# Performance work log

Hardware: AMD Instinct MI355X
Metric: run time of the kernel (lower is better)

The kernel has to match this reference:

```python
import jax, jax.numpy as jnp
import numpy as np

B, L, S, D, H, CTX = 2, 2048, 512, 1024, 16, 1024
HD = D // H
HID = 4 * D
EPS = 1e-6


def _ln(x):
    mu = jnp.mean(x, axis=-1, keepdims=True)
    var = jnp.mean((x - mu) ** 2, axis=-1, keepdims=True)
    return (x - mu) * jax.lax.rsqrt(var + EPS)


def _rotate_half(x):
    x1, x2 = jnp.split(x, 2, axis=-1)
    return jnp.concatenate([-x2, x1], axis=-1)


def _heads(t):  # [B,N,D] -> [B,H,N,HD]
    return t.reshape(t.shape[0], t.shape[1], H, HD).transpose(0, 2, 1, 3)


def _merge(t):  # [B,H,N,HD] -> [B,N,D]
    return t.transpose(0, 2, 1, 3).reshape(t.shape[0], t.shape[2], D)


def setup_inputs() -> dict:
    key = jax.random.key(0)
    ks = jax.random.split(key, 24)
    s = 0.02
    inp = {
        "x": jax.random.normal(ks[0], (B, L, D), jnp.float32),
        "timestep_emb": jax.random.normal(ks[1], (B, D), jnp.float32),
        "context_emb": jax.random.normal(ks[2], (B, S, CTX), jnp.float32),
        "rope_emb": jax.random.normal(ks[3], (L, HD), jnp.float32),
        # adaLN modulation: Linear(D -> 6D) with bias
        "w_mod": jax.random.normal(ks[4], (D, 6 * D), jnp.float32) * s,
        "b_mod": jnp.zeros((6 * D,), jnp.float32),
        # self-attention (no qkv bias, out has bias)
        "wq_s": jax.random.normal(ks[5], (D, D), jnp.float32) * s,
        "wk_s": jax.random.normal(ks[6], (D, D), jnp.float32) * s,
        "wv_s": jax.random.normal(ks[7], (D, D), jnp.float32) * s,
        "wo_s": jax.random.normal(ks[8], (D, D), jnp.float32) * s,
        "bo_s": jnp.zeros((D,), jnp.float32),
        # cross-attention (q/k/v no bias, out has bias)
        "wq_c": jax.random.normal(ks[9], (D, D), jnp.float32) * s,
        "wk_c": jax.random.normal(ks[10], (CTX, D), jnp.float32) * s,
        "wv_c": jax.random.normal(ks[11], (CTX, D), jnp.float32) * s,
        "wo_c": jax.random.normal(ks[12], (D, D), jnp.float32) * s,
        "bo_c": jnp.zeros((D,), jnp.float32),
        # MLP
        "w1": jax.random.normal(ks[13], (D, HID), jnp.float32) * s,
        "b1": jnp.zeros((HID,), jnp.float32),
        "w2": jax.random.normal(ks[14], (HID, D), jnp.float32) * s,
        "b2": jnp.zeros((D,), jnp.float32),
    }
    return inp


def reference(x, timestep_emb, context_emb, rope_emb,
              w_mod, b_mod,
              wq_s, wk_s, wv_s, wo_s, bo_s,
              wq_c, wk_c, wv_c, wo_c, bo_c,
              w1, b1, w2, b2):
    scale = HD ** -0.5
    # adaLN modulation from timestep embedding
    mods = jnp.split(timestep_emb @ w_mod + b_mod, 6, axis=-1)
    shift_msa, scale_msa, gate_msa, shift_mlp, scale_mlp, gate_mlp = mods

    # --- self-attention with RoPE ---
    nx = _ln(x) * (1.0 + scale_msa[:, None, :]) + shift_msa[:, None, :]
    q = _heads(nx @ wq_s)
    k = _heads(nx @ wk_s)
    v = _heads(nx @ wv_s)
    cos = jnp.cos(rope_emb)[None, None]  # [1,1,L,HD]
    sin = jnp.sin(rope_emb)[None, None]
    q = q * cos + _rotate_half(q) * sin
    k = k * cos + _rotate_half(k) * sin
    attn = jax.nn.softmax(jnp.einsum("bhqd,bhkd->bhqk", q, k) * scale, axis=-1)
    sa = _merge(jnp.einsum("bhqk,bhkd->bhqd", attn, v)) @ wo_s + bo_s
    x = x + gate_msa[:, None, :] * sa

    # --- cross-attention (no mask) ---
    nx = _ln(x)
    q = _heads(nx @ wq_c)
    k = _heads(context_emb @ wk_c)
    v = _heads(context_emb @ wv_c)
    attn = jax.nn.softmax(jnp.einsum("bhqd,bhkd->bhqk", q, k) * scale, axis=-1)
    ca = _merge(jnp.einsum("bhqk,bhkd->bhqd", attn, v)) @ wo_c + bo_c
    x = x + ca

    # --- MLP with modulation + gate ---
    nx = _ln(x) * (1.0 + scale_mlp[:, None, :]) + shift_mlp[:, None, :]
    h = jax.nn.gelu(nx @ w1 + b1, approximate=False)
    x = x + gate_mlp[:, None, :] * (h @ w2 + b2)
    return x
```

## Files before the change

kernel.cpp:

```cpp
#include <hip/hip_runtime.h>
#include <hip/hip_bf16.h>


typedef short short8 __attribute__((ext_vector_type(8)));
typedef float f32x4 __attribute__((ext_vector_type(4)));
typedef float f32x16 __attribute__((ext_vector_type(16)));

#define DEV __device__ __forceinline__

DEV unsigned short f2b(float f) {
  __hip_bfloat16 h = __float2bfloat16(f);
  return *reinterpret_cast<unsigned short*>(&h);
}
DEV float b2f(unsigned short u) {
  unsigned int x = ((unsigned int)u) << 16;
  return __builtin_bit_cast(float, x);
}
DEV unsigned int pk2(float lo, float hi) {
  unsigned int r;
  asm("v_cvt_pk_bf16_f32 %0, %1, %2" : "=v"(r) : "v"(lo), "v"(hi));
  return r;
}
DEV void vpsw(unsigned int& a, unsigned int& b) {
  asm("v_permlane32_swap_b32 %0, %1" : "+v"(a), "+v"(b));
}
DEV float max3f(float a, float b, float c) {
  float r;
  asm("v_max3_f32 %0, %1, %2, %3" : "=v"(r) : "v"(a), "v"(b), "v"(c));
  return r;
}

#define GLB(p) ((const __attribute__((address_space(1))) void*)(p))
#define LDSP(p) ((__attribute__((address_space(3))) void*)(p))

__global__ __launch_bounds__(256) void transpose_cast(
    const float* __restrict__ in, unsigned short* __restrict__ out, int R, int C,
    float scale) {
  __shared__ float tile[32][33];
  int bx = blockIdx.x * 32, by = blockIdx.y * 32;
  int tx = threadIdx.x, ty = threadIdx.y;
#pragma unroll
  for (int i = ty; i < 32; i += 8)
    tile[i][tx] = in[(size_t)(by + i) * C + bx + tx];
  __syncthreads();
#pragma unroll
  for (int i = ty; i < 32; i += 8)
    out[(size_t)(bx + i) * R + by + tx] = f2b(tile[tx][i] * scale);
}

struct TCB { const float* in; unsigned short* out; float scale; };
struct TC8 { TCB m[8]; };
__global__ __launch_bounds__(256) void transpose_cast8(TC8 a) {
  __shared__ float tile[32][33];
  const float* in = a.m[blockIdx.z].in;
  unsigned short* out = a.m[blockIdx.z].out;
  float scale = a.m[blockIdx.z].scale;
  int bx = blockIdx.x * 32, by = blockIdx.y * 32;
  int tx = threadIdx.x, ty = threadIdx.y;
#pragma unroll
  for (int i = ty; i < 32; i += 8)
    tile[i][tx] = in[(size_t)(by + i) * 1024 + bx + tx];
  __syncthreads();
#pragma unroll
  for (int i = ty; i < 32; i += 8)
    out[(size_t)(bx + i) * 1024 + by + tx] = f2b(tile[tx][i] * scale);
}

__global__ __launch_bounds__(256) void cast_bf16(
    const float* __restrict__ in, unsigned short* __restrict__ out, int n) {
  int i = blockIdx.x * 256 + threadIdx.x;
  if (i < n) out[i] = f2b(in[i]);
}

__global__ __launch_bounds__(256) void rope_tab(
    const float* __restrict__ rope, float* __restrict__ cosT, float* __restrict__ sinT, int n) {
  int i = blockIdx.x * 256 + threadIdx.x;
  if (i < n) {
    float v = rope[i];
    cosT[i] = cosf(v);
    sinT[i] = sinf(v);
  }
}

__global__ __launch_bounds__(256) void mods_kernel(
    const float* __restrict__ te, const unsigned short* __restrict__ wmodT,
    const float* __restrict__ bmod, float* __restrict__ mods) {
  int w = blockIdx.x * 4 + (threadIdx.x >> 6);
  int lane = threadIdx.x & 63;
  int b = w / 6144, j = w % 6144;
  const unsigned short* wr = wmodT + (size_t)j * 1024;
  const float* ter = te + (size_t)b * 1024;
  int k0 = lane * 16;
  float sum = 0.f;
#pragma unroll
  for (int u = 0; u < 2; ++u) {
    short8 wv = *(const short8*)(wr + k0 + u * 8);
#pragma unroll
    for (int e = 0; e < 8; ++e)
      sum += b2f((unsigned short)wv[e]) * ter[k0 + u * 8 + e];
  }
#pragma unroll
  for (int off = 32; off >= 1; off >>= 1) sum += __shfl_down(sum, off);
  if (lane == 0) mods[(size_t)b * 6144 + j] = sum + bmod[j];
}

__global__ __launch_bounds__(256) void ln_mod(
    const float* __restrict__ x, const float* __restrict__ mods,
    unsigned short* __restrict__ out, int scale_ofs, int shift_ofs) {
  int row = blockIdx.x;
  int b = row >> 11;
  int tid = threadIdx.x;
  const float* xr = x + (size_t)row * 1024;
  float4 v = ((const float4*)xr)[tid];
  float s = v.x + v.y + v.z + v.w;
  float ss = v.x * v.x + v.y * v.y + v.z * v.z + v.w * v.w;
#pragma unroll
  for (int off = 32; off >= 1; off >>= 1) {
    s += __shfl_down(s, off);
    ss += __shfl_down(ss, off);
  }
  __shared__ float red[8];
  int wave = tid >> 6, lane = tid & 63;
  if (lane == 0) { red[wave] = s; red[4 + wave] = ss; }
  __syncthreads();
  if (tid == 0) {
    float S = red[0] + red[1] + red[2] + red[3];
    float SS = red[4] + red[5] + red[6] + red[7];
    float mu = S * (1.f / 1024.f);
    red[0] = mu;
    red[1] = SS * (1.f / 1024.f) - mu * mu;
  }
  __syncthreads();
  float mu = red[0];
  float rs = rsqrtf(red[1] + 1e-6f);
  float vv[4] = {v.x, v.y, v.z, v.w};
  unsigned short o[4];
#pragma unroll
  for (int c = 0; c < 4; ++c) {
    int col = tid * 4 + c;
    float nv = (vv[c] - mu) * rs;
    if (scale_ofs >= 0)
      nv = nv * (1.f + mods[(size_t)b * 6144 + scale_ofs + col]) +
           mods[(size_t)b * 6144 + shift_ofs + col];
    o[c] = f2b(nv);
  }
  *(ushort4*)(&out[(size_t)row * 1024 + tid * 4]) = *(const ushort4*)o;
}

__global__ __launch_bounds__(256) void rope_apply(
    unsigned short* __restrict__ qb, unsigned short* __restrict__ kb,
    const float* __restrict__ cosT, const float* __restrict__ sinT) {
  int idx = blockIdx.x * 256 + threadIdx.x;
  unsigned short* buf = blockIdx.y ? kb : qb;
  int row = idx >> 9;
  int rem = idx & 511;
  int h = rem >> 5, d = rem & 31;
  int l = row & 2047;
  size_t base = (size_t)row * 1024 + h * 64 + d;
  float x1 = b2f(buf[base]), x2 = b2f(buf[base + 32]);
  float c1 = cosT[l * 64 + d], s1 = sinT[l * 64 + d];
  float c2 = cosT[l * 64 + d + 32], s2 = sinT[l * 64 + d + 32];
  buf[base] = f2b(x1 * c1 - x2 * s1);
  buf[base + 32] = f2b(x2 * c2 + x1 * s2);
}

template <int EPI, int MI, int NJ>
DEV void gemm_epilogue(f32x4 (&acc)[MI][NJ], void* Cout, const float* bias,
                       const float* mods, int gate_ofs, const float* src,
                       int N, int rowsPerB, int m0, int n0, int wm, int wn,
                       int g, int r) {
#pragma unroll
  for (int i = 0; i < MI; ++i) {
#pragma unroll
    for (int j = 0; j < NJ; ++j) {
#pragma unroll
      for (int q = 0; q < 4; ++q) {
        size_t grow = (size_t)(m0 + wm + i * 16 + g * 4 + q);
        size_t gcol = (size_t)(n0 + wn + j * 16 + r);
        float v = acc[i][j][q];
        if constexpr (EPI == 0) {
          ((unsigned short*)Cout)[grow * N + gcol] = f2b(v);
        } else if constexpr (EPI == 1) {
          v += bias[gcol];
          float ge = 0.5f * v * (1.0f + erff(v * 0.70710678f));
          ((unsigned short*)Cout)[grow * N + gcol] = f2b(ge);
        } else if constexpr (EPI == 3) {
          size_t buf = gcol >> 10;
          ((unsigned short*)Cout)[buf * (4096ull * 1024) + grow * 1024 + (gcol & 1023)] = f2b(v);
        } else {
          v += bias[gcol];
          float gate = 1.0f;
          if (gate_ofs >= 0)
            gate = mods[(grow / rowsPerB) * 6144 + gate_ofs + gcol];
          ((float*)Cout)[grow * N + gcol] = src[grow * N + gcol] + gate * v;
        }
      }
    }
  }
}

template <int EPI>
__global__ __launch_bounds__(256, 2) void gemm_bt(
    const unsigned short* __restrict__ A, const unsigned short* __restrict__ Bt,
    void* __restrict__ Cout, const float* __restrict__ bias,
    const float* __restrict__ mods, int gate_ofs, const float* __restrict__ src,
    int M, int N, int K, int rowsPerB) {
  __shared__ unsigned short As[128 * 32];
  __shared__ unsigned short Bs[128 * 32];
  const int tid = threadIdx.x;
  const int wave = tid >> 6, lane = tid & 63;
  const int g = lane >> 4, r = lane & 15;
  const int m0 = blockIdx.y * 128, n0 = blockIdx.x * 128;
  const int wm = (wave >> 1) * 64, wn = (wave & 1) * 64;
  const int srow = lane >> 2;
  const int scol = (lane & 3) * 8;

  f32x4 acc[4][4] = {};

  for (int k0 = 0; k0 < K; k0 += 32) {
    __syncthreads();
#pragma unroll
    for (int cc = 0; cc < 4; ++cc) {
      int c = wave * 4 + cc;
      int isB = c >> 3;
      int cl = c & 7;
      int row = cl * 16 + srow;
      const unsigned short* gsrc =
          isB ? (Bt + (size_t)(n0 + row) * K + k0 + scol)
              : (A + (size_t)(m0 + row) * K + k0 + scol);
      unsigned short* ldst = (isB ? Bs : As) + cl * 512;
      __builtin_amdgcn_global_load_lds(GLB(gsrc), LDSP(ldst), 16, 0, 0);
    }
    __syncthreads();

    short8 bfr[4];
#pragma unroll
    for (int j = 0; j < 4; ++j)
      bfr[j] = *(const short8*)(&Bs[(wn + j * 16 + r) * 32 + g * 8]);
#pragma unroll
    for (int i = 0; i < 4; ++i) {
      short8 af = *(const short8*)(&As[(wm + i * 16 + r) * 32 + g * 8]);
#pragma unroll
      for (int j = 0; j < 4; ++j)
        acc[i][j] = __builtin_amdgcn_mfma_f32_16x16x32_bf16(af, bfr[j], acc[i][j], 0, 0, 0);
    }
  }
  gemm_epilogue<EPI, 4, 4>(acc, Cout, bias, mods, gate_ofs, src, N, rowsPerB,
                           m0, n0, wm, wn, g, r);
}

template <int EPI>
__global__ __launch_bounds__(256) void gemm_pipe(
    const unsigned short* __restrict__ A, const unsigned short* __restrict__ Bt,
    void* __restrict__ Cout, const float* __restrict__ bias,
    const float* __restrict__ mods, int gate_ofs, const float* __restrict__ src,
    int M, int N, int K, int rowsPerB, int mshift) {
  __shared__ unsigned short lds[4 * 16384];
  const int tid = threadIdx.x;
  const int wave = tid >> 6, lane = tid & 63;
  const int g = lane >> 4, r = lane & 15;
  const int flat = blockIdx.x;
  const int xcd = flat & 7, idx = flat >> 3;
  const int mt = xcd * (1 << mshift) + (idx & ((1 << mshift) - 1));
  const int nt = idx >> mshift;
  const int m0 = mt * 128, n0 = nt * 128;
  const int wm = (wave >> 1) * 64, wn = (wave & 1) * 64;
  const int srow8 = lane >> 3;
  const int sck = (lane & 7) ^ srow8;

  f32x4 acc[4][4] = {};

  auto stage = [&](int t, int bufi) {
    const int k0 = t * 64;
#pragma unroll
    for (int i = 0; i < 8; ++i) {
      int u = wave * 8 + i;
      int isB = u >> 4;
      int uu = u & 15;
      int rl = uu * 8 + srow8;
      const unsigned short* gsrc =
          (isB ? (Bt + (size_t)(n0 + rl) * K) : (A + (size_t)(m0 + rl) * K)) +
          k0 + sck * 8;
      unsigned short* dst = (unsigned short*)lds + bufi * 16384 + isB * 8192 + uu * 512;
      __builtin_amdgcn_global_load_lds(GLB(gsrc), LDSP(dst), 16, 0, 0);
    }
  };

  const int nt_k = K / 64;
  stage(0, 0);
  stage(1, 1);
  stage(2, 2);

  for (int t = 0; t < nt_k; ++t) {
    int rem = nt_k - t;
    if (rem >= 3) {
      asm volatile("s_waitcnt vmcnt(16)" ::: "memory");
    } else if (rem == 2) {
      asm volatile("s_waitcnt vmcnt(8)" ::: "memory");
    } else {
      asm volatile("s_waitcnt vmcnt(0)" ::: "memory");
    }
    __builtin_amdgcn_sched_barrier(0);
    __builtin_amdgcn_s_barrier();
    __builtin_amdgcn_sched_barrier(0);
    if (t + 3 < nt_k) stage(t + 3, (t + 3) & 3);

    const unsigned short* Ab = (const unsigned short*)lds + (t & 3) * 16384;
    const unsigned short* Bb = Ab + 8192;
#pragma unroll
    for (int ks = 0; ks < 2; ++ks) {
      short8 bfr[4];
#pragma unroll
      for (int j = 0; j < 4; ++j) {
        int row = wn + j * 16 + r;
        bfr[j] = *(const short8*)&Bb[row * 64 + ((g + ks * 4) ^ (r & 7)) * 8];
      }
#pragma unroll
      for (int i = 0; i < 4; ++i) {
        int row = wm + i * 16 + r;
        short8 af = *(const short8*)&Ab[row * 64 + ((g + ks * 4) ^ (r & 7)) * 8];
#pragma unroll
        for (int j = 0; j < 4; ++j)
          acc[i][j] = __builtin_amdgcn_mfma_f32_16x16x32_bf16(af, bfr[j], acc[i][j], 0, 0, 0);
      }
    }
  }
  gemm_epilogue<EPI, 4, 4>(acc, Cout, bias, mods, gate_ofs, src, N, rowsPerB,
                           m0, n0, wm, wn, g, r);
}

template <int EPI>
__global__ __launch_bounds__(256) void gemm_p2(
    const unsigned short* __restrict__ A, const unsigned short* __restrict__ Bt,
    void* __restrict__ Cout, const float* __restrict__ bias,
    const float* __restrict__ mods, int gate_ofs, const float* __restrict__ src,
    int M, int N, int K, int rowsPerB, int ntn) {
  __shared__ unsigned short lds[3 * 12288];
  const int tid = threadIdx.x;
  const int wave = tid >> 6, lane = tid & 63;
  const int g = lane >> 4, r = lane & 15;
  const int flat = blockIdx.x;
  const int nt = flat % ntn, mt = flat / ntn;
  const int m0 = mt * 64, n0 = nt * 128;
  const int wm = (wave >> 1) * 32, wn = (wave & 1) * 64;
  const int srow8 = lane >> 3;
  const int sck = (lane & 7) ^ srow8;

  f32x4 acc[2][4] = {};

  auto stage = [&](int t, int bufi) {
    const int k0 = t * 64;
    unsigned short* base = (unsigned short*)lds + bufi * 12288;
#pragma unroll
    for (int i = 0; i < 2; ++i) {
      int u = wave * 2 + i;
      int rl = u * 8 + srow8;
      const unsigned short* gsrc = A + (size_t)(m0 + rl) * K + k0 + sck * 8;
      __builtin_amdgcn_global_load_lds(GLB(gsrc), LDSP(base + u * 512), 16, 0, 0);
    }
#pragma unroll
    for (int i = 0; i < 4; ++i) {
      int u = wave * 4 + i;
      int rl = u * 8 + srow8;
      const unsigned short* gsrc = Bt + (size_t)(n0 + rl) * K + k0 + sck * 8;
      __builtin_amdgcn_global_load_lds(GLB(gsrc), LDSP(base + 4096 + u * 512), 16, 0, 0);
    }
  };

  const int ntk = K / 64;
  stage(0, 0);
  stage(1, 1);
  int cbuf = 0, sbuf = 2;

  for (int t = 0; t < ntk; ++t) {
    if (t < ntk - 1) {
      asm volatile("s_waitcnt vmcnt(6)" ::: "memory");
    } else {
      asm volatile("s_waitcnt vmcnt(0)" ::: "memory");
    }
    __builtin_amdgcn_sched_barrier(0);
    __builtin_amdgcn_s_barrier();
    __builtin_amdgcn_sched_barrier(0);
    if (t + 2 < ntk) {
      stage(t + 2, sbuf);
      sbuf = (sbuf == 2) ? 0 : sbuf + 1;
    }

    const unsigned short* Ab = (const unsigned short*)lds + cbuf * 12288;
    const unsigned short* Bb = Ab + 4096;
#pragma unroll
    for (int ks = 0; ks < 2; ++ks) {
      short8 bfr[4];
#pragma unroll
      for (int j = 0; j < 4; ++j) {
        int row = wn + j * 16 + r;
        bfr[j] = *(const short8*)&Bb[row * 64 + ((g + ks * 4) ^ (r & 7)) * 8];
      }
#pragma unroll
      for (int i = 0; i < 2; ++i) {
        int row = wm + i * 16 + r;
        short8 af = *(const short8*)&Ab[row * 64 + ((g + ks * 4) ^ (r & 7)) * 8];
#pragma unroll
        for (int j = 0; j < 4; ++j)
          acc[i][j] = __builtin_amdgcn_mfma_f32_16x16x32_bf16(af, bfr[j], acc[i][j], 0, 0, 0);
      }
    }
    cbuf = (cbuf == 2) ? 0 : cbuf + 1;
  }
  gemm_epilogue<EPI, 2, 4>(acc, Cout, bias, mods, gate_ofs, src, N, rowsPerB,
                           m0, n0, wm, wn, g, r);
}

__global__ __launch_bounds__(256, 2) void flash2(
    const unsigned short* __restrict__ Q, const unsigned short* __restrict__ Kv,
    const unsigned short* __restrict__ Vv, unsigned short* __restrict__ O,
    int Lk) {
  __shared__ unsigned short lds[20480];
  const int tid = threadIdx.x, wave = tid >> 6, lane = tid & 63;
  const int hi = lane >> 5, lq = lane & 31;
  const int flat = blockIdx.x;
  const int xcd = flat & 7, rr = flat >> 3;
  const int gl = rr >> 4, qt = rr & 15;
  const int g = xcd * 4 + gl;
  const int h = g & 15, b = g >> 4;
  const int Lq = 2048, D = 1024;

  const unsigned short* Qbase =
      Q + ((size_t)b * Lq + qt * 128 + wave * 32 + lq) * D + h * 64;
  const unsigned short* Kbase = Kv + (size_t)b * Lk * D + h * 64;
  const unsigned short* Vbase = Vv + (size_t)b * Lk * D + h * 64;

  short8 qf[4];
#pragma unroll
  for (int kb = 0; kb < 4; ++kb)
    qf[kb] = *(const short8*)(Qbase + kb * 16 + hi * 8);

  const short8 ones = {0x3F80, 0x3F80, 0x3F80, 0x3F80, 0x3F80, 0x3F80, 0x3F80, 0x3F80};

  const int kr0 = tid >> 3, kc0 = tid & 7;
  const int kvp = tid >> 3, db = tid & 7;
  const int kch0 = (kc0 ^ (kr0 & 7) ^ (kr0 >> 3)) & 7;
  const int kch1 = kch0 ^ 4;
  const int f0 = (lq & 7) ^ (lq >> 3);
  const int swz0 = f0 << 4, swz1 = swz0 ^ 64;

  int vby[8];
#pragma unroll
  for (int e = 0; e < 8; ++e) {
    int d = db * 8 + e;
    vby[e] = d * 128 + ((kvp * 4) ^ (((e ^ db) & 7) << 4));
  }

  float m_run = -3.0e38f;
  f32x16 o0 = {}, o1 = {}, lacc = {};
  short8 vr0, vr1;
  short8 pbf[4];

  auto stageK = [&](int t, int bi) {
    const unsigned short* s0 = Kbase + (size_t)(t * 64 + kr0) * D + kch0 * 8;
    const unsigned short* s1 = Kbase + (size_t)(t * 64 + kr0 + 32) * D + kch1 * 8;
    __builtin_amdgcn_global_load_lds(GLB(s0), LDSP(&lds[bi * 4096 + wave * 512]), 16, 0, 0);
    __builtin_amdgcn_global_load_lds(GLB(s1), LDSP(&lds[bi * 4096 + 2048 + wave * 512]), 16, 0, 0);
  };
  auto loadV = [&](int t) {
    const unsigned short* v0 = Vbase + (size_t)(t * 64 + 2 * kvp) * D + db * 8;
    vr0 = *(const short8*)v0;
    vr1 = *(const short8*)(v0 + D);
  };
  auto writeV = [&](int t) {
    char* vt = (char*)&lds[12288 + (t & 1) * 4096];
#pragma unroll
    for (int e = 0; e < 8; ++e)
      *(unsigned int*)(vt + vby[e]) =
          (unsigned int)(unsigned short)vr0[e] |
          ((unsigned int)(unsigned short)vr1[e] << 16);
  };
  auto qk = [&](int bi, f32x16& sa0, f32x16& sa1) {
    const unsigned short* K0 = &lds[bi * 4096];
#pragma unroll
    for (int ks = 0; ks < 4; ++ks) {
      int lo = ks * 32 + hi * 16;
      short8 a0 = *(const short8*)&K0[lq * 64 + ((lo ^ swz0) >> 1)];
      short8 a1 = *(const short8*)&K0[(32 + lq) * 64 + ((lo ^ swz1) >> 1)];
      sa0 = __builtin_amdgcn_mfma_f32_32x32x16_bf16(a0, qf[ks], sa0, 0, 0, 0);
      sa1 = __builtin_amdgcn_mfma_f32_32x32x16_bf16(a1, qf[ks], sa1, 0, 0, 0);
    }
  };
  auto finish = [&](f32x16& s0a, f32x16& s1a) {
    float tm[8];
#pragma unroll
    for (int i = 0; i < 8; ++i)
      tm[i] = fmaxf(max3f(s0a[i], s0a[i + 8], s1a[i]), s1a[i + 8]);
    float x = max3f(tm[0], tm[1], tm[2]);
    float y = max3f(tm[3], tm[4], tm[5]);
    float pm = fmaxf(max3f(tm[6], tm[7], x), y);
    {
      unsigned int ua = __builtin_bit_cast(unsigned int, pm), ub = ua;
      vpsw(ua, ub);
      pm = fmaxf(__builtin_bit_cast(float, ua), __builtin_bit_cast(float, ub));
    }
    if (__any(pm - m_run > 8.0f)) {
      float mnew = fmaxf(m_run, pm);
      float alpha = exp2f(m_run - mnew);
      lacc[0] *= alpha;
#pragma unroll
      for (int i = 0; i < 16; ++i) { o0[i] *= alpha; o1[i] *= alpha; }
      m_run = mnew;
    }
    float mc = m_run;
#pragma unroll
    for (int i = 0; i < 16; ++i) s0a[i] = exp2f(s0a[i] - mc);
#pragma unroll
    for (int i = 0; i < 16; ++i) s1a[i] = exp2f(s1a[i] - mc);
#pragma unroll
    for (int kb = 0; kb < 4; ++kb) {
      int bb = (kb & 1) * 8;
      float p0, p1, p2, p3, p4, p5, p6, p7;
      if (kb < 2) {
        p0 = s0a[bb + 0]; p1 = s0a[bb + 1]; p2 = s0a[bb + 2]; p3 = s0a[bb + 3];
        p4 = s0a[bb + 4]; p5 = s0a[bb + 5]; p6 = s0a[bb + 6]; p7 = s0a[bb + 7];
      } else {
        p0 = s1a[bb + 0]; p1 = s1a[bb + 1]; p2 = s1a[bb + 2]; p3 = s1a[bb + 3];
        p4 = s1a[bb + 4]; p5 = s1a[bb + 5]; p6 = s1a[bb + 6]; p7 = s1a[bb + 7];
      }
      unsigned int u0 = pk2(p0, p1), u1 = pk2(p2, p3);
      unsigned int u2 = pk2(p4, p5), u3 = pk2(p6, p7);
      vpsw(u0, u2);
      vpsw(u1, u3);
      union { unsigned int u[4]; short8 s; } fr;
      fr.u[0] = u0; fr.u[1] = u1; fr.u[2] = u2; fr.u[3] = u3;
      pbf[kb] = fr.s;
    }
  };
  auto pv = [&](int t) {
    const unsigned short* V0 = &lds[12288 + (t & 1) * 4096];
    __builtin_amdgcn_s_setprio(1);
#pragma unroll
    for (int kb = 0; kb < 4; ++kb) {
      int lo = kb * 32 + hi * 16;
      short8 vf0 = *(const short8*)&V0[lq * 64 + ((lo ^ swz0) >> 1)];
      short8 vf1 = *(const short8*)&V0[(32 + lq) * 64 + ((lo ^ swz1) >> 1)];
      o0 = __builtin_amdgcn_mfma_f32_32x32x16_bf16(vf0, pbf[kb], o0, 0, 0, 0);
      o1 = __builtin_amdgcn_mfma_f32_32x32x16_bf16(vf1, pbf[kb], o1, 0, 0, 0);
      lacc = __builtin_amdgcn_mfma_f32_32x32x16_bf16(ones, pbf[kb], lacc, 0, 0, 0);
    }
    __builtin_amdgcn_s_setprio(0);
  };

  const int nkt = Lk / 64;

  stageK(0, 0);
  loadV(0);
  writeV(0);
  stageK(1, 1);
  __syncthreads();

  f32x16 sA0 = {}, sA1 = {}, sB0, sB1;
  qk(0, sA0, sA1);

  auto pstep = [&](int t, f32x16& n0, f32x16& n1, f32x16& p0, f32x16& p1) {
    const int tq = t + 1;
    if (tq < nkt) {
      loadV(tq);
      if (tq + 1 < nkt) stageK(tq + 1, (tq + 1) % 3);
      n0 = {}; n1 = {};
      qk(tq % 3, n0, n1);
    }
    finish(p0, p1);
    if (tq < nkt) writeV(tq);
    pv(t);
    __syncthreads();
  };

  for (int t = 0; t < nkt; t += 2) {
    pstep(t, sB0, sB1, sA0, sA1);
    pstep(t + 1, sA0, sA1, sB0, sB1);
  }

  float rl = 1.0f / lacc[0];
  unsigned short* os = &lds[wave * 2048];
#pragma unroll
  for (int t = 0; t < 2; ++t) {
#pragma unroll
    for (int c = 0; c < 4; ++c) {
      int dbase = 32 * t + 8 * c + 4 * hi;
      float v0 = (t ? o1[4 * c + 0] : o0[4 * c + 0]) * rl;
      float v1 = (t ? o1[4 * c + 1] : o0[4 * c + 1]) * rl;
      float v2 = (t ? o1[4 * c + 2] : o0[4 * c + 2]) * rl;
      float v3 = (t ? o1[4 * c + 3] : o0[4 * c + 3]) * rl;
      int by0 = lq * 128 + ((dbase * 2) ^ ((lq & 7) << 4));
      int by1 = lq * 128 + (((dbase + 2) * 2) ^ ((lq & 7) << 4));
      *(unsigned int*)((char*)os + by0) = pk2(v0, v1);
      *(unsigned int*)((char*)os + by1) = pk2(v2, v3);
    }
  }
  int q2 = lane >> 1;
  unsigned short* orow =
      O + ((size_t)b * Lq + qt * 128 + wave * 32 + q2) * D + h * 64;
#pragma unroll
  for (int j = 0; j < 4; ++j) {
    int j2 = (lane & 1) * 4 + j;
    int byr = q2 * 128 + ((j2 * 16) ^ ((q2 & 7) << 4));
    short8 vv = *(const short8*)((char*)os + byr);
    *(short8*)(orow + j2 * 8) = vv;
  }
}

extern "C" void kernel_launch(void* const* d_in, const int* in_sizes, int n_in,
                              void* d_out, int out_size, void* d_ws, size_t ws_size,
                              hipStream_t stream) {
  (void)in_sizes; (void)n_in; (void)out_size; (void)ws_size;
  const float* x_in = (const float*)d_in[0];
  const float* te   = (const float*)d_in[1];
  const float* ctx  = (const float*)d_in[2];
  const float* rope = (const float*)d_in[3];
  const float* wmod = (const float*)d_in[4];
  const float* bmod = (const float*)d_in[5];
  const float* wqs  = (const float*)d_in[6];
  const float* wks  = (const float*)d_in[7];
  const float* wvs  = (const float*)d_in[8];
  const float* wos  = (const float*)d_in[9];
  const float* bos  = (const float*)d_in[10];
  const float* wqc  = (const float*)d_in[11];
  const float* wkc  = (const float*)d_in[12];
  const float* wvc  = (const float*)d_in[13];
  const float* woc  = (const float*)d_in[14];
  const float* boc  = (const float*)d_in[15];
  const float* w1   = (const float*)d_in[16];
  const float* b1   = (const float*)d_in[17];
  const float* w2   = (const float*)d_in[18];
  const float* b2   = (const float*)d_in[19];
  float* out = (float*)d_out;

  char* w = (char*)d_ws;
  size_t o = 0;
  auto alloc = [&](size_t bytes) {
    char* p = w + o;
    o = (o + bytes + 255) & ~(size_t)255;
    return p;
  };
  unsigned short* wmodT = (unsigned short*)alloc(6144ull * 1024 * 2);
  unsigned short* wqsT  = (unsigned short*)alloc(1024ull * 1024 * 2);
  unsigned short* wksT  = (unsigned short*)alloc(1024ull * 1024 * 2);
  unsigned short* wvsT  = (unsigned short*)alloc(1024ull * 1024 * 2);
  unsigned short* wosT  = (unsigned short*)alloc(1024ull * 1024 * 2);
  unsigned short* wqcT  = (unsigned short*)alloc(1024ull * 1024 * 2);
  unsigned short* wkcT  = (unsigned short*)alloc(1024ull * 1024 * 2);
  unsigned short* wvcT  = (unsigned short*)alloc(1024ull * 1024 * 2);
  unsigned short* wocT  = (unsigned short*)alloc(1024ull * 1024 * 2);
  unsigned short* w1T   = (unsigned short*)alloc(4096ull * 1024 * 2);
  unsigned short* w2T   = (unsigned short*)alloc(1024ull * 4096 * 2);
  float* modsb = (float*)alloc(2ull * 6144 * 4);
  float* cosT  = (float*)alloc(2048ull * 64 * 4);
  float* sinT  = (float*)alloc(2048ull * 64 * 4);
  unsigned short* nx   = (unsigned short*)alloc(4096ull * 1024 * 2);
  unsigned short* ctxb = (unsigned short*)alloc(1024ull * 1024 * 2);
  unsigned short* qb = (unsigned short*)alloc(4096ull * 1024 * 2);
  unsigned short* kb = (unsigned short*)alloc(4096ull * 1024 * 2);
  unsigned short* vb = (unsigned short*)alloc(4096ull * 1024 * 2);
  unsigned short* ao = (unsigned short*)alloc(4096ull * 1024 * 2);
  float* xw = (float*)alloc(4096ull * 1024 * 4);
  unsigned short* hbuf = qb;

  const float c1 = 0.125f * 1.4426950408889634f;

  dim3 tb(32, 8);
  transpose_cast<<<dim3(6144 / 32, 1024 / 32), tb, 0, stream>>>(wmod, wmodT, 1024, 6144, 1.0f);
  TC8 tc8;
  tc8.m[0] = {wqs, wqsT, c1};
  tc8.m[1] = {wks, wksT, 1.0f};
  tc8.m[2] = {wvs, wvsT, 1.0f};
  tc8.m[3] = {wos, wosT, 1.0f};
  tc8.m[4] = {wqc, wqcT, 1.0f};
  tc8.m[5] = {wkc, wkcT, c1};
  tc8.m[6] = {wvc, wvcT, 1.0f};
  tc8.m[7] = {woc, wocT, 1.0f};
  transpose_cast8<<<dim3(32, 32, 8), tb, 0, stream>>>(tc8);
  transpose_cast<<<dim3(4096 / 32, 1024 / 32), tb, 0, stream>>>(w1, w1T, 1024, 4096, 1.0f);
  transpose_cast<<<dim3(1024 / 32, 4096 / 32), tb, 0, stream>>>(w2, w2T, 4096, 1024, 1.0f);

  cast_bf16<<<4096, 256, 0, stream>>>(ctx, ctxb, 1024 * 1024);
  rope_tab<<<512, 256, 0, stream>>>(rope, cosT, sinT, 2048 * 64);
  mods_kernel<<<3072, 256, 0, stream>>>(te, wmodT, bmod, modsb);

  ln_mod<<<4096, 256, 0, stream>>>(x_in, modsb, nx, 1024, 0);
  gemm_pipe<3><<<768, 256, 0, stream>>>(nx, wqsT, qb, nullptr, nullptr, -1, nullptr, 4096, 3072, 1024, 2048, 2);
  rope_apply<<<dim3(8192, 2), 256, 0, stream>>>(qb, kb, cosT, sinT);
  flash2<<<512, 256, 0, stream>>>(qb, kb, vb, ao, 2048);
  gemm_p2<2><<<512, 256, 0, stream>>>(ao, wosT, xw, bos, modsb, 2048, x_in, 4096, 1024, 1024, 2048, 8);

  ln_mod<<<4096, 256, 0, stream>>>(xw, modsb, nx, -1, -1);
  gemm_p2<0><<<512, 256, 0, stream>>>(nx, wqcT, qb, nullptr, nullptr, -1, nullptr, 4096, 1024, 1024, 2048, 8);
  gemm_p2<3><<<256, 256, 0, stream>>>(ctxb, wkcT, kb, nullptr, nullptr, -1, nullptr, 1024, 2048, 1024, 512, 16);
  flash2<<<512, 256, 0, stream>>>(qb, kb, vb, ao, 512);
  gemm_p2<2><<<512, 256, 0, stream>>>(ao, wocT, xw, boc, modsb, -1, xw, 4096, 1024, 1024, 2048, 8);

  ln_mod<<<4096, 256, 0, stream>>>(xw, modsb, nx, 4096, 3072);
  gemm_bt<1><<<dim3(32, 32), 256, 0, stream>>>(nx, w1T, hbuf, b1, nullptr, -1, nullptr, 4096, 4096, 1024, 2048);
  gemm_p2<2><<<512, 256, 0, stream>>>(hbuf, w2T, out, b2, modsb, 5120, xw, 4096, 1024, 4096, 2048, 8);
}
```

Baseline: 409.9 us.

## Fuse RoPE into QKV GEMM epilogue and trim flash-attention accumulator init

New measurement: 401.1 us. 2.2% less time.

```diff
diff --git a/kernel.cpp b/kernel.cpp
--- a/kernel.cpp
+++ b/kernel.cpp
@@ -73,12 +73,11 @@
 }
 
 __global__ __launch_bounds__(256) void rope_tab(
-    const float* __restrict__ rope, float* __restrict__ cosT, float* __restrict__ sinT, int n) {
+    const float* __restrict__ rope, float2* __restrict__ cs, int n) {
   int i = blockIdx.x * 256 + threadIdx.x;
   if (i < n) {
     float v = rope[i];
-    cosT[i] = cosf(v);
-    sinT[i] = sinf(v);
+    cs[i] = make_float2(cosf(v), sinf(v));
   }
 }
 
@@ -145,23 +144,6 @@
     o[c] = f2b(nv);
   }
   *(ushort4*)(&out[(size_t)row * 1024 + tid * 4]) = *(const ushort4*)o;
-}
-
-__global__ __launch_bounds__(256) void rope_apply(
-    unsigned short* __restrict__ qb, unsigned short* __restrict__ kb,
-    const float* __restrict__ cosT, const float* __restrict__ sinT) {
-  int idx = blockIdx.x * 256 + threadIdx.x;
-  unsigned short* buf = blockIdx.y ? kb : qb;
-  int row = idx >> 9;
-  int rem = idx & 511;
-  int h = rem >> 5, d = rem & 31;
-  int l = row & 2047;
-  size_t base = (size_t)row * 1024 + h * 64 + d;
-  float x1 = b2f(buf[base]), x2 = b2f(buf[base + 32]);
-  float c1 = cosT[l * 64 + d], s1 = sinT[l * 64 + d];
-  float c2 = cosT[l * 64 + d + 32], s2 = sinT[l * 64 + d + 32];
-  buf[base] = f2b(x1 * c1 - x2 * s1);
-  buf[base + 32] = f2b(x2 * c2 + x1 * s2);
 }
 
 template <int EPI, int MI, int NJ>
@@ -199,6 +181,37 @@
   }
 }
 
+DEV void qkv_rope_epilogue(f32x4 (&acc)[4][4], unsigned short* Cout,
+                           const float2* cs, int m0, int n0, int wm, int wn,
+                           int g, int r) {
+  const int buf = (n0 + wn) >> 10;
+  const int colbase = (n0 + wn) & 1023;
+  unsigned short* base = Cout + (size_t)buf * (4096ull * 1024);
+#pragma unroll
+  for (int i = 0; i < 4; ++i) {
+#pragma unroll
+    for (int q = 0; q < 4; ++q) {
+      size_t grow = (size_t)(m0 + wm + i * 16 + g * 4 + q);
+      unsigned short* orow = base + grow * 1024 + colbase + r;
+      if (buf < 2) {
+        int l = (int)(grow & 2047);
+#pragma unroll
+        for (int j = 0; j < 2; ++j) {
+          int d = j * 16 + r;
+          float2 a = cs[l * 64 + d];
+          float2 bb = cs[l * 64 + d + 32];
+          float x1 = acc[i][j][q], x2 = acc[i][j + 2][q];
+          orow[j * 16] = f2b(x1 * a.x - x2 * a.y);
+          orow[(j + 2) * 16] = f2b(x2 * bb.x + x1 * bb.y);
+        }
+      } else {
+#pragma unroll
+        for (int j = 0; j < 4; ++j) orow[j * 16] = f2b(acc[i][j][q]);
+      }
+    }
+  }
+}
+
 template <int EPI>
 __global__ __launch_bounds__(256, 2) void gemm_bt(
     const unsigned short* __restrict__ A, const unsigned short* __restrict__ Bt,
@@ -325,8 +338,13 @@
       }
     }
   }
-  gemm_epilogue<EPI, 4, 4>(acc, Cout, bias, mods, gate_ofs, src, N, rowsPerB,
-                           m0, n0, wm, wn, g, r);
+  if constexpr (EPI == 4) {
+    qkv_rope_epilogue(acc, (unsigned short*)Cout, (const float2*)bias,
+                      m0, n0, wm, wn, g, r);
+  } else {
+    gemm_epilogue<EPI, 4, 4>(acc, Cout, bias, mods, gate_ofs, src, N, rowsPerB,
+                             m0, n0, wm, wn, g, r);
+  }
 }
 
 template <int EPI>
@@ -436,6 +454,7 @@
     qf[kb] = *(const short8*)(Qbase + kb * 16 + hi * 8);
 
   const short8 ones = {0x3F80, 0x3F80, 0x3F80, 0x3F80, 0x3F80, 0x3F80, 0x3F80, 0x3F80};
+  const f32x16 z16 = {};
 
   const int kr0 = tid >> 3, kc0 = tid & 7;
   const int kvp = tid >> 3, db = tid & 7;
@@ -469,16 +488,27 @@
   };
   auto writeV = [&](int t) {
     char* vt = (char*)&lds[12288 + (t & 1) * 4096];
-#pragma unroll
-    for (int e = 0; e < 8; ++e)
-      *(unsigned int*)(vt + vby[e]) =
-          (unsigned int)(unsigned short)vr0[e] |
-          ((unsigned int)(unsigned short)vr1[e] << 16);
+    union { short8 s; unsigned int u[4]; } a, c;
+    a.s = vr0; c.s = vr1;
+#pragma unroll
+    for (int k = 0; k < 4; ++k) {
+      *(unsigned int*)(vt + vby[2 * k]) =
+          __builtin_amdgcn_perm(c.u[k], a.u[k], 0x05040100u);
+      *(unsigned int*)(vt + vby[2 * k + 1]) =
+          __builtin_amdgcn_perm(c.u[k], a.u[k], 0x07060302u);
+    }
   };
   auto qk = [&](int bi, f32x16& sa0, f32x16& sa1) {
     const unsigned short* K0 = &lds[bi * 4096];
-#pragma unroll
-    for (int ks = 0; ks < 4; ++ks) {
+    {
+      int lo = hi * 16;
+      short8 a0 = *(const short8*)&K0[lq * 64 + ((lo ^ swz0) >> 1)];
+      short8 a1 = *(const short8*)&K0[(32 + lq) * 64 + ((lo ^ swz1) >> 1)];
+      sa0 = __builtin_amdgcn_mfma_f32_32x32x16_bf16(a0, qf[0], z16, 0, 0, 0);
+      sa1 = __builtin_amdgcn_mfma_f32_32x32x16_bf16(a1, qf[0], z16, 0, 0, 0);
+    }
+#pragma unroll
+    for (int ks = 1; ks < 4; ++ks) {
       int lo = ks * 32 + hi * 16;
       short8 a0 = *(const short8*)&K0[lq * 64 + ((lo ^ swz0) >> 1)];
       short8 a1 = *(const short8*)&K0[(32 + lq) * 64 + ((lo ^ swz1) >> 1)];
@@ -555,7 +585,7 @@
   stageK(1, 1);
   __syncthreads();
 
-  f32x16 sA0 = {}, sA1 = {}, sB0, sB1;
+  f32x16 sA0, sA1, sB0, sB1;
   qk(0, sA0, sA1);
 
   auto pstep = [&](int t, f32x16& n0, f32x16& n1, f32x16& p0, f32x16& p1) {
@@ -563,7 +593,6 @@
     if (tq < nkt) {
       loadV(tq);
       if (tq + 1 < nkt) stageK(tq + 1, (tq + 1) % 3);
-      n0 = {}; n1 = {};
       qk(tq % 3, n0, n1);
     }
     finish(p0, p1);
@@ -651,8 +680,7 @@
   unsigned short* w1T   = (unsigned short*)alloc(4096ull * 1024 * 2);
   unsigned short* w2T   = (unsigned short*)alloc(1024ull * 4096 * 2);
   float* modsb = (float*)alloc(2ull * 6144 * 4);
-  float* cosT  = (float*)alloc(2048ull * 64 * 4);
-  float* sinT  = (float*)alloc(2048ull * 64 * 4);
+  float2* csT  = (float2*)alloc(2048ull * 64 * 8);
   unsigned short* nx   = (unsigned short*)alloc(4096ull * 1024 * 2);
   unsigned short* ctxb = (unsigned short*)alloc(1024ull * 1024 * 2);
   unsigned short* qb = (unsigned short*)alloc(4096ull * 1024 * 2);
@@ -680,12 +708,11 @@
   transpose_cast<<<dim3(1024 / 32, 4096 / 32), tb, 0, stream>>>(w2, w2T, 4096, 1024, 1.0f);
 
   cast_bf16<<<4096, 256, 0, stream>>>(ctx, ctxb, 1024 * 1024);
-  rope_tab<<<512, 256, 0, stream>>>(rope, cosT, sinT, 2048 * 64);
+  rope_tab<<<512, 256, 0, stream>>>(rope, csT, 2048 * 64);
   mods_kernel<<<3072, 256, 0, stream>>>(te, wmodT, bmod, modsb);
 
   ln_mod<<<4096, 256, 0, stream>>>(x_in, modsb, nx, 1024, 0);
-  gemm_pipe<3><<<768, 256, 0, stream>>>(nx, wqsT, qb, nullptr, nullptr, -1, nullptr, 4096, 3072, 1024, 2048, 2);
-  rope_apply<<<dim3(8192, 2), 256, 0, stream>>>(qb, kb, cosT, sinT);
+  gemm_pipe<4><<<768, 256, 0, stream>>>(nx, wqsT, qb, (const float*)csT, nullptr, -1, nullptr, 4096, 3072, 1024, 2048, 2);
   flash2<<<512, 256, 0, stream>>>(qb, kb, vb, ao, 2048);
   gemm_p2<2><<<512, 256, 0, stream>>>(ao, wosT, xw, bos, modsb, 2048, x_in, 4096, 1024, 1024, 2048, 8);
 
```
